# Kernel optimization log

Hardware: AMD Instinct MI355X
Metric: run time of the kernel (lower is better)

Reference implementation:

```python
import jax, jax.numpy as jnp
import numpy as np

N = 50000      # nodes
DEG = 12       # in-degree per node
E = N * DEG    # 600000 edges
IN_FEATS = 256
H_FEATS = 128
NUM_LAYERS = 2
BN_EPS = 1e-5
PD_EPS = 1e-6  # torch pairwise_distance eps


def _batch_norm(x):
    # BatchNorm1d(affine=False) in training mode: per-feature batch stats, biased var
    m = x.mean(axis=0)
    v = ((x - m) ** 2).mean(axis=0)
    return (x - m) / jnp.sqrt(v + BN_EPS)


def setup_inputs() -> dict:
    key = jax.random.key(0)
    ks = jax.random.split(key, 6)
    x = jax.random.normal(ks[0], (N, IN_FEATS), dtype=jnp.float32)
    # xavier-uniform-like scales
    s_init = float(np.sqrt(6.0 / (IN_FEATS + H_FEATS)))
    s_h = float(np.sqrt(6.0 / (2 * H_FEATS)))
    W_init = jax.random.uniform(ks[1], (IN_FEATS, H_FEATS), jnp.float32, -s_init, s_init)
    W0 = jax.random.uniform(ks[2], (H_FEATS, H_FEATS), jnp.float32, -s_h, s_h)
    W1 = jax.random.uniform(ks[3], (H_FEATS, H_FEATS), jnp.float32, -s_h, s_h)
    b0 = jnp.zeros((H_FEATS,), jnp.float32)
    b1 = jnp.zeros((H_FEATS,), jnp.float32)
    src = jax.random.randint(ks[4], (E,), 0, N, dtype=jnp.int32)
    dst = jnp.repeat(jnp.arange(N, dtype=jnp.int32), DEG)  # every node has in-degree DEG
    return {"x": x, "W_init": W_init, "W0": W0, "b0": b0, "W1": W1, "b1": b1,
            "src": src, "dst": dst}


def _embed_nodes(x, W_init, Ws, bs, src, dst):
    # h = act(norm(x @ init_weight)); then GraphConv(norm='none') layers
    h = jax.nn.relu(_batch_norm(x @ W_init))
    for W, b in zip(Ws, bs):
        msg = h[src] @ W                       # [E, H]
        agg = jax.ops.segment_sum(msg, dst, num_segments=N)  # sum aggregation
        h = jax.nn.relu(_batch_norm(agg + b))
    return h


def _nonparametric_embedding(x, src, dst, deg):
    # GIN(apply_func=None, eps=-1, aggregator='mean') == mean of in-neighbors
    h = jax.nn.relu(_batch_norm(x))
    for _ in range(NUM_LAYERS):
        agg = jax.ops.segment_sum(h[src], dst, num_segments=N) / deg[:, None]
        h = jax.nn.relu(_batch_norm(agg))
    return h


def _mean_edge_dist(h, src, dst, deg):
    # apply_edges: pairwise_distance(src, dst); pull: scatter-mean onto dst
    d = jnp.linalg.norm(h[src] - h[dst] + PD_EPS, axis=1)  # [E]
    return jax.ops.segment_sum(d, dst, num_segments=N) / deg  # [N]


def reference(x, W_init, W0, b0, W1, b1, src, dst):
    deg = jnp.maximum(
        jax.ops.segment_sum(jnp.ones((E,), jnp.float32), dst, num_segments=N), 1.0)
    h_final = _embed_nodes(x, W_init, (W0, W1), (b0, b1), src, dst)
    # nonparametric target distances (detached in original)
    h_nonpar = _nonparametric_embedding(jax.lax.stop_gradient(x), src, dst, deg)
    d_nonpar = jax.lax.stop_gradient(_mean_edge_dist(h_nonpar, src, dst, deg))
    d_par = _mean_edge_dist(h_final, src, dst, deg)
    loss = jnp.mean((jnp.log(d_par) - jnp.log(d_nonpar)) ** 2)
    return (h_final, loss)
```

## Files before the change

### kernel.cpp

```cpp
#include <hip/hip_runtime.h>
#include <hip/hip_fp16.h>
#include <math.h>

#define DEG 12
#define BN_EPS 1e-5f
#define PD_EPS 1e-6f

using uint = unsigned int;

typedef _Float16 fp16x8 __attribute__((ext_vector_type(8)));
typedef float f32x2 __attribute__((ext_vector_type(2)));
typedef float f32x4 __attribute__((ext_vector_type(4)));

__device__ inline float2 h2f2(uint u) {
  __half2 h; __builtin_memcpy(&h, &u, 4);
  return __half22float2(h);
}
__device__ inline uint f2h2(float a, float b) {
  __half2 h = __floats2half2_rn(a, b);
  uint u; __builtin_memcpy(&u, &h, 4);
  return u;
}
__device__ inline f32x2 q2f_lo(uint u) { return __builtin_amdgcn_cvt_pk_f32_fp8(u, false); }
__device__ inline f32x2 q2f_hi(uint u) { return __builtin_amdgcn_cvt_pk_f32_fp8(u, true); }
__device__ inline uint f4_to_q(float a, float b, float c, float d) {
  uint w = 0;
  w = __builtin_amdgcn_cvt_pk_fp8_f32(a, b, w, false);
  w = __builtin_amdgcn_cvt_pk_fp8_f32(c, d, w, true);
  return w;
}

#define STATS_NB 256

template<int F>
__global__ __launch_bounds__(512) void stats_h_part(const __half* __restrict__ in,
                                                    float* __restrict__ parts, int M) {
  const int G = F / 8;
  __shared__ float redA[512 * 8];
  __shared__ float redB[512 * 8];
  int tid = threadIdx.x;
  int total = M * G;
  float s[8] = {0,0,0,0,0,0,0,0}, q[8] = {0,0,0,0,0,0,0,0};
  for (int i = blockIdx.x * 512 + tid; i < total; i += gridDim.x * 512) {
    uint4 raw = ((const uint4*)in)[i];
    float2 v0 = h2f2(raw.x), v1 = h2f2(raw.y), v2 = h2f2(raw.z), v3 = h2f2(raw.w);
    float v[8] = {v0.x, v0.y, v1.x, v1.y, v2.x, v2.y, v3.x, v3.y};
#pragma unroll
    for (int j = 0; j < 8; ++j) { s[j] += v[j]; q[j] += v[j] * v[j]; }
  }
#pragma unroll
  for (int j = 0; j < 8; ++j) { redA[tid * 8 + j] = s[j]; redB[tid * 8 + j] = q[j]; }
  __syncthreads();
  if (tid < F) {
    int c = tid >> 3, j = tid & 7;
    float as = 0.f, aq = 0.f;
#pragma unroll 4
    for (int r = 0; r < 512 / G; ++r) {
      as += redA[(r * G + c) * 8 + j];
      aq += redB[(r * G + c) * 8 + j];
    }
    parts[blockIdx.x * 2 * F + tid]     = as;
    parts[blockIdx.x * 2 * F + F + tid] = aq;
  }
}

template<int F>
__global__ __launch_bounds__(512) void stats_q_part(const uint* __restrict__ in,
                                                    float* __restrict__ parts, int M) {
  const int G = F / 8;
  __shared__ float redA[512 * 8];
  __shared__ float redB[512 * 8];
  int tid = threadIdx.x;
  int total = M * G;
  float s[8] = {0,0,0,0,0,0,0,0}, q[8] = {0,0,0,0,0,0,0,0};
  for (int i = blockIdx.x * 512 + tid; i < total; i += gridDim.x * 512) {
    uint2 raw = ((const uint2*)in)[i];
    f32x2 a = q2f_lo(raw.x), b = q2f_hi(raw.x), c = q2f_lo(raw.y), d = q2f_hi(raw.y);
    float v[8] = {a.x, a.y, b.x, b.y, c.x, c.y, d.x, d.y};
#pragma unroll
    for (int j = 0; j < 8; ++j) { s[j] += v[j]; q[j] += v[j] * v[j]; }
  }
#pragma unroll
  for (int j = 0; j < 8; ++j) { redA[tid * 8 + j] = s[j]; redB[tid * 8 + j] = q[j]; }
  __syncthreads();
  if (tid < F) {
    int c = tid >> 3, j = tid & 7;
    float as = 0.f, aq = 0.f;
#pragma unroll 4
    for (int r = 0; r < 512 / G; ++r) {
      as += redA[(r * G + c) * 8 + j];
      aq += redB[(r * G + c) * 8 + j];
    }
    parts[blockIdx.x * 2 * F + tid]     = as;
    parts[blockIdx.x * 2 * F + F + tid] = aq;
  }
}

template<int F>
__global__ __launch_bounds__(512) void stats_f_part(const float* __restrict__ in,
                                                    float* __restrict__ parts, int M) {
  const int G = F / 4;
  __shared__ float redA[512 * 4];
  __shared__ float redB[512 * 4];
  int tid = threadIdx.x;
  int total = M * G;
  float s[4] = {0,0,0,0}, q[4] = {0,0,0,0};
  for (int i = blockIdx.x * 512 + tid; i < total; i += gridDim.x * 512) {
    float4 v = ((const float4*)in)[i];
    float w[4] = {v.x, v.y, v.z, v.w};
#pragma unroll
    for (int j = 0; j < 4; ++j) { s[j] += w[j]; q[j] += w[j] * w[j]; }
  }
#pragma unroll
  for (int j = 0; j < 4; ++j) { redA[tid * 4 + j] = s[j]; redB[tid * 4 + j] = q[j]; }
  __syncthreads();
  if (tid < F) {
    int c = tid >> 2, j = tid & 3;
    float as = 0.f, aq = 0.f;
#pragma unroll 4
    for (int r = 0; r < 512 / G; ++r) {
      as += redA[(r * G + c) * 4 + j];
      aq += redB[(r * G + c) * 4 + j];
    }
    parts[blockIdx.x * 2 * F + tid]     = as;
    parts[blockIdx.x * 2 * F + F + tid] = aq;
  }
}

template<int F>
__global__ __launch_bounds__(1024) void stats_final(const float* __restrict__ parts,
                                                    int M, float* __restrict__ stats) {
  const int OUT = 2 * F;
  const int T   = 1024 / OUT;
  __shared__ float red[1024];
  int tid = threadIdx.x;
  int o = tid & (OUT - 1);
  int c = tid / OUT;
  float s = 0.f;
#pragma unroll 16
  for (int b = c; b < STATS_NB; b += T) s += parts[b * OUT + o];
  red[tid] = s;
  __syncthreads();
  if (tid < OUT) {
    float acc = red[tid];
#pragma unroll
    for (int cc = 1; cc < T; ++cc) acc += red[cc * OUT + tid];
    red[tid] = acc;
  }
  __syncthreads();
  if (tid < F) {
    float mean = red[tid] / (float)M;
    float var  = red[F + tid] / (float)M - mean * mean;
    stats[tid]     = mean;
    stats[F + tid] = 1.0f / sqrtf(var + BN_EPS);
  }
}

__global__ void transpose_cast(const float* __restrict__ W, __half* __restrict__ WT, int K) {
  int idx = blockIdx.x * 256 + threadIdx.x;
  if (idx >= 128 * K) return;
  int n = idx / K, k = idx - n * K;
  WT[idx] = __float2half(W[(size_t)k * 128 + n]);
}

__global__ __launch_bounds__(256) void gemm_x(
    const float* __restrict__ A, const __half* __restrict__ WT,
    __half* __restrict__ C, int M) {
  int wave = threadIdx.x >> 6, lane = threadIdx.x & 63;
  int row0 = blockIdx.x * 64 + wave * 16;
  if (row0 >= M) return;
  int r  = lane & 15;
  int kg = lane >> 4;
  const float* Ap = A + (size_t)(row0 + r) * 256 + kg * 8;

  fp16x8 af[8];
#pragma unroll
  for (int a = 0; a < 8; ++a) {
    float4 lo = *(const float4*)(Ap + a * 32);
    float4 hi = *(const float4*)(Ap + a * 32 + 4);
    af[a][0] = (_Float16)lo.x; af[a][1] = (_Float16)lo.y;
    af[a][2] = (_Float16)lo.z; af[a][3] = (_Float16)lo.w;
    af[a][4] = (_Float16)hi.x; af[a][5] = (_Float16)hi.y;
    af[a][6] = (_Float16)hi.z; af[a][7] = (_Float16)hi.w;
  }
  f32x4 acc[8];
#pragma unroll
  for (int n = 0; n < 8; ++n) acc[n] = (f32x4){0.f, 0.f, 0.f, 0.f};
  const _Float16* WTh = (const _Float16*)WT;
#pragma unroll
  for (int a = 0; a < 8; ++a) {
#pragma unroll
    for (int n = 0; n < 8; ++n) {
      fp16x8 bf = *(const fp16x8*)(WTh + (size_t)(n * 16 + r) * 256 + kg * 8 + a * 32);
      acc[n] = __builtin_amdgcn_mfma_f32_16x16x32_f16(af[a], bf, acc[n], 0, 0, 0);
    }
  }
#pragma unroll
  for (int n = 0; n < 8; ++n) {
    int col = n * 16 + r;
#pragma unroll
    for (int rr = 0; rr < 4; ++rr) {
      int row = row0 + kg * 4 + rr;
      if (row < M) C[(size_t)row * 128 + col] = __float2half(acc[n][rr]);
    }
  }
}

template<bool OUT_HALF>
__global__ __launch_bounds__(256) void gemm_128(
    const __half* __restrict__ A, const __half* __restrict__ WT,
    const float* __restrict__ bias, void* __restrict__ Cv, int M) {
  int wave = threadIdx.x >> 6, lane = threadIdx.x & 63;
  int row0 = blockIdx.x * 64 + wave * 16;
  if (row0 >= M) return;
  int r  = lane & 15;
  int kg = lane >> 4;
  const _Float16* Ap = (const _Float16*)A + (size_t)(row0 + r) * 128 + kg * 8;

  fp16x8 af[4];
#pragma unroll
  for (int a = 0; a < 4; ++a) af[a] = *(const fp16x8*)(Ap + a * 32);

  f32x4 acc[8];
#pragma unroll
  for (int n = 0; n < 8; ++n) acc[n] = (f32x4){0.f, 0.f, 0.f, 0.f};
  const _Float16* WTh = (const _Float16*)WT;
#pragma unroll
  for (int a = 0; a < 4; ++a) {
#pragma unroll
    for (int n = 0; n < 8; ++n) {
      fp16x8 bf = *(const fp16x8*)(WTh + (size_t)(n * 16 + r) * 128 + kg * 8 + a * 32);
      acc[n] = __builtin_amdgcn_mfma_f32_16x16x32_f16(af[a], bf, acc[n], 0, 0, 0);
    }
  }
#pragma unroll
  for (int n = 0; n < 8; ++n) {
    int col = n * 16 + r;
    float bv = bias[col];
#pragma unroll
    for (int rr = 0; rr < 4; ++rr) {
      int row = row0 + kg * 4 + rr;
      if (row >= M) continue;
      float v = acc[n][rr] + bv;
      if (OUT_HALF) ((__half*)Cv)[(size_t)row * 128 + col] = __float2half(v);
      else          ((float*)Cv)[(size_t)row * 128 + col] = v;
    }
  }
}

template<int F, bool BNRELU>
__global__ __launch_bounds__(256) void agg_n(
    const __half* __restrict__ H, const float* __restrict__ stats,
    const int* __restrict__ src, __half* __restrict__ outh,
    float scale, int n_nodes) {
  const int LPN = F / 8;
  const int NPB = 256 / LPN;
  int tid  = threadIdx.x;
  int g    = tid / LPN;
  int lig  = tid % LPN;
  int node = blockIdx.x * NPB + g;
  if (node >= n_nodes) return;
  float m[8], iv[8];
  if (BNRELU) {
#pragma unroll
    for (int j = 0; j < 8; ++j) {
      m[j]  = stats[lig * 8 + j];
      iv[j] = stats[F + lig * 8 + j];
    }
  }
  int lane = tid & 63;
  int grpStart = lane & (63 ^ (LPN - 1));
  int se = 0;
  if ((lane & (LPN - 1)) < DEG) se = src[node * DEG + (lane & (LPN - 1))];

  const uint4* HH = (const uint4*)H;
  float a[8] = {0,0,0,0,0,0,0,0};
#pragma unroll
  for (int e = 0; e < DEG; ++e) {
    int s = __shfl(se, grpStart + e);
    uint4 raw = HH[(size_t)s * LPN + lig];
    float2 v0 = h2f2(raw.x), v1 = h2f2(raw.y), v2 = h2f2(raw.z), v3 = h2f2(raw.w);
    float w[8] = {v0.x, v0.y, v1.x, v1.y, v2.x, v2.y, v3.x, v3.y};
    if (BNRELU) {
#pragma unroll
      for (int j = 0; j < 8; ++j) w[j] = fmaxf((w[j] - m[j]) * iv[j], 0.f);
    }
#pragma unroll
    for (int j = 0; j < 8; ++j) a[j] += w[j];
  }
  uint4 w;
  w.x = f2h2(a[0] * scale, a[1] * scale);
  w.y = f2h2(a[2] * scale, a[3] * scale);
  w.z = f2h2(a[4] * scale, a[5] * scale);
  w.w = f2h2(a[6] * scale, a[7] * scale);
  ((uint4*)outh)[(size_t)node * LPN + lig] = w;
}

template<int F, bool BNRELU>
__global__ __launch_bounds__(256) void agg_q(
    const uint* __restrict__ H, const float* __restrict__ stats,
    const int* __restrict__ src, uint* __restrict__ outq,
    float scale, int n_nodes) {
  const int LPN = F / 8;
  const int NPB = 256 / LPN;
  int tid  = threadIdx.x;
  int g    = tid / LPN;
  int lig  = tid % LPN;
  int node = blockIdx.x * NPB + g;
  if (node >= n_nodes) return;
  float m[8], iv[8];
  if (BNRELU) {
#pragma unroll
    for (int j = 0; j < 8; ++j) {
      m[j]  = stats[lig * 8 + j];
      iv[j] = stats[F + lig * 8 + j];
    }
  }
  int lane = tid & 63;
  int grpStart = lane & (63 ^ (LPN - 1));
  int se = 0;
  if ((lane & (LPN - 1)) < DEG) se = src[node * DEG + (lane & (LPN - 1))];

  const uint2* HH = (const uint2*)H;
  float a[8] = {0,0,0,0,0,0,0,0};
#pragma unroll
  for (int e = 0; e < DEG; ++e) {
    int s = __shfl(se, grpStart + e);
    uint2 raw = HH[(size_t)s * LPN + lig];
    f32x2 p0 = q2f_lo(raw.x), p1 = q2f_hi(raw.x), p2 = q2f_lo(raw.y), p3 = q2f_hi(raw.y);
    float w[8] = {p0.x, p0.y, p1.x, p1.y, p2.x, p2.y, p3.x, p3.y};
    if (BNRELU) {
#pragma unroll
      for (int j = 0; j < 8; ++j) w[j] = fmaxf((w[j] - m[j]) * iv[j], 0.f);
    }
#pragma unroll
    for (int j = 0; j < 8; ++j) a[j] += w[j];
  }
  uint2 w;
  w.x = f4_to_q(a[0] * scale, a[1] * scale, a[2] * scale, a[3] * scale);
  w.y = f4_to_q(a[4] * scale, a[5] * scale, a[6] * scale, a[7] * scale);
  ((uint2*)outq)[(size_t)node * LPN + lig] = w;
}

template<int F>
__global__ __launch_bounds__(256) void dist_q(
    const uint* __restrict__ H, const int* __restrict__ src,
    float* __restrict__ out, int n_nodes) {
  const int LPN = 16;
  const int NPB = 256 / LPN;
  const int NU2 = F / 128;
  int tid  = threadIdx.x;
  int g    = tid / LPN;
  int lig  = tid % LPN;
  int node = blockIdx.x * NPB + g;
  if (node >= n_nodes) return;
  int lane = tid & 63;
  int grpStart = lane & 48;
  int se = 0;
  if ((lane & 15) < DEG) se = src[node * DEG + (lane & 15)];

  const uint2* HH = (const uint2*)H;
  float oe[NU2 * 8];
#pragma unroll
  for (int k = 0; k < NU2; ++k) {
    uint2 o = HH[(size_t)node * (F / 8) + lig * NU2 + k];
    f32x2 p0 = q2f_lo(o.x), p1 = q2f_hi(o.x), p2 = q2f_lo(o.y), p3 = q2f_hi(o.y);
    oe[k*8+0] = PD_EPS - p0.x; oe[k*8+1] = PD_EPS - p0.y;
    oe[k*8+2] = PD_EPS - p1.x; oe[k*8+3] = PD_EPS - p1.y;
    oe[k*8+4] = PD_EPS - p2.x; oe[k*8+5] = PD_EPS - p2.y;
    oe[k*8+6] = PD_EPS - p3.x; oe[k*8+7] = PD_EPS - p3.y;
  }

  float dsum = 0.f;
#pragma unroll
  for (int e = 0; e < DEG; ++e) {
    int s = __shfl(se, grpStart + e);
    float sq = 0.f;
#pragma unroll
    for (int k = 0; k < NU2; ++k) {
      uint2 raw = HH[(size_t)s * (F / 8) + lig * NU2 + k];
      f32x2 p0 = q2f_lo(raw.x), p1 = q2f_hi(raw.x), p2 = q2f_lo(raw.y), p3 = q2f_hi(raw.y);
      float w[8] = {p0.x, p0.y, p1.x, p1.y, p2.x, p2.y, p3.x, p3.y};
#pragma unroll
      for (int j = 0; j < 8; ++j) {
        float d = w[j] + oe[k*8+j];
        sq = fmaf(d, d, sq);
      }
    }
#pragma unroll
    for (int mask = 1; mask < LPN; mask <<= 1) sq += __shfl_xor(sq, mask);
    dsum += sqrtf(sq);
  }
  if (lig == 0) out[node] = dsum * (1.0f / (float)DEG);
}

template<int F>
__global__ void bnrelu_to_fp8(const float* __restrict__ in, const float* __restrict__ stats,
                              uint* __restrict__ out, int total4) {
  for (int idx = blockIdx.x * blockDim.x + threadIdx.x; idx < total4;
       idx += gridDim.x * blockDim.x) {
    float4 v = ((const float4*)in)[idx];
    int f0 = (idx & (F / 4 - 1)) * 4;
    float w0 = fmaxf((v.x - stats[f0+0]) * stats[F+f0+0], 0.f);
    float w1 = fmaxf((v.y - stats[f0+1]) * stats[F+f0+1], 0.f);
    float w2 = fmaxf((v.z - stats[f0+2]) * stats[F+f0+2], 0.f);
    float w3 = fmaxf((v.w - stats[f0+3]) * stats[F+f0+3], 0.f);
    out[idx] = f4_to_q(w0, w1, w2, w3);
  }
}

template<int F>
__global__ void bnrelu_q2q(const uint* __restrict__ in, const float* __restrict__ stats,
                           uint* __restrict__ out, int total1) {
  for (int idx = blockIdx.x * blockDim.x + threadIdx.x; idx < total1;
       idx += gridDim.x * blockDim.x) {
    uint raw = in[idx];
    int f0 = (idx & (F / 4 - 1)) * 4;
    f32x2 p0 = q2f_lo(raw), p1 = q2f_hi(raw);
    float w0 = fmaxf((p0.x - stats[f0+0]) * stats[F+f0+0], 0.f);
    float w1 = fmaxf((p0.y - stats[f0+1]) * stats[F+f0+1], 0.f);
    float w2 = fmaxf((p1.x - stats[f0+2]) * stats[F+f0+2], 0.f);
    float w3 = fmaxf((p1.y - stats[f0+3]) * stats[F+f0+3], 0.f);
    out[idx] = f4_to_q(w0, w1, w2, w3);
  }
}

template<int F>
__global__ void bnrelu_dual(const float* __restrict__ in, const float* __restrict__ stats,
                            float* __restrict__ outf, uint* __restrict__ outq, int total4) {
  for (int idx = blockIdx.x * blockDim.x + threadIdx.x; idx < total4;
       idx += gridDim.x * blockDim.x) {
    float4 v = ((const float4*)in)[idx];
    int f0 = (idx & (F / 4 - 1)) * 4;
    float w0 = fmaxf((v.x - stats[f0+0]) * stats[F+f0+0], 0.f);
    float w1 = fmaxf((v.y - stats[f0+1]) * stats[F+f0+1], 0.f);
    float w2 = fmaxf((v.z - stats[f0+2]) * stats[F+f0+2], 0.f);
    float w3 = fmaxf((v.w - stats[f0+3]) * stats[F+f0+3], 0.f);
    ((float4*)outf)[idx] = make_float4(w0, w1, w2, w3);
    outq[idx] = f4_to_q(w0, w1, w2, w3);
  }
}

__global__ void loss_partial(const float* __restrict__ dpar, const float* __restrict__ dnp,
                             float* __restrict__ parts, int n) {
  __shared__ float red[256];
  float acc = 0.f;
  for (int i = blockIdx.x * 256 + threadIdx.x; i < n; i += gridDim.x * 256) {
    float t = logf(dpar[i]) - logf(dnp[i]);
    acc += t * t;
  }
  red[threadIdx.x] = acc;
  __syncthreads();
  for (int s = 128; s; s >>= 1) {
    if (threadIdx.x < s) red[threadIdx.x] += red[threadIdx.x + s];
    __syncthreads();
  }
  if (threadIdx.x == 0) parts[blockIdx.x] = red[0];
}

__global__ void loss_final(const float* __restrict__ parts, int nb,
                           float* __restrict__ out, float inv_n) {
  if (threadIdx.x == 0) {
    float s = 0.f;
    for (int i = 0; i < nb; ++i) s += parts[i];
    *out = s * inv_n;
  }
}

extern "C" void kernel_launch(void* const* d_in, const int* in_sizes, int n_in,
                              void* d_out, int out_size, void* d_ws, size_t ws_size,
                              hipStream_t stream) {
  const float* x  = (const float*)d_in[0];
  const float* Wi = (const float*)d_in[1];
  const float* W0 = (const float*)d_in[2];
  const float* b0 = (const float*)d_in[3];
  const float* W1 = (const float*)d_in[4];
  const float* b1 = (const float*)d_in[5];
  const int*  src = (const int*)d_in[6];

  const int N = in_sizes[0] / 256;
  float* out = (float*)d_out;

  const size_t NF = (size_t)N * 128;
  float* S1 = (float*)d_ws;
  float* S2 = S1 + NF;
  float* S3 = S2 + NF;
  float* aux = S3 + NF;
  float* dpar   = aux;
  float* dnp    = dpar + N;
  float* parts  = dnp + N;
  float* s_x    = parts + STATS_NB * 512;
  float* s_y0   = s_x + 512;
  float* s_z1   = s_y0 + 256;
  float* s_z2   = s_z1 + 256;
  float* s_a1   = s_z2 + 256;
  float* s_a2   = s_a1 + 512;
  float* lparts = s_a2 + 512;
  __half* WiT   = (__half*)(lparts + 64);
  __half* W0T   = (__half*)(lparts + 64 + 16384);
  __half* W1T   = (__half*)(lparts + 64 + 24576);

  __half* y0h = (__half*)S1;
  __half* H0h = (__half*)S2;
  __half* z1h = (__half*)S1;
  __half* H1h = (__half*)S2;
  float*  z2  = S3;
  uint* hq   = (uint*)S1;
  uint* xq   = (uint*)S2;
  uint* A1q  = (uint*)S3;
  uint* A2q  = (uint*)S2;
  uint* A2nq = (uint*)S1;

  const int g64   = (N + 63) / 64;
  const int g128a = N / 16;
  const int gaggq = N / 8;
  const int gdist = N / 16;

  transpose_cast<<<(128 * 256 + 255) / 256, 256, 0, stream>>>(Wi, WiT, 256);
  transpose_cast<<<(128 * 128 + 255) / 256, 256, 0, stream>>>(W0, W0T, 128);
  transpose_cast<<<(128 * 128 + 255) / 256, 256, 0, stream>>>(W1, W1T, 128);

  gemm_x<<<g64, 256, 0, stream>>>(x, WiT, y0h, N);
  stats_h_part<128><<<STATS_NB, 512, 0, stream>>>(y0h, parts, N);
  stats_final<128><<<1, 1024, 0, stream>>>(parts, N, s_y0);
  agg_n<128, true><<<g128a, 256, 0, stream>>>(y0h, s_y0, src, H0h, 1.0f, N);
  gemm_128<true><<<g64, 256, 0, stream>>>(H0h, W0T, b0, z1h, N);
  stats_h_part<128><<<STATS_NB, 512, 0, stream>>>(z1h, parts, N);
  stats_final<128><<<1, 1024, 0, stream>>>(parts, N, s_z1);
  agg_n<128, true><<<g128a, 256, 0, stream>>>(z1h, s_z1, src, H1h, 1.0f, N);
  gemm_128<false><<<g64, 256, 0, stream>>>(H1h, W1T, b1, z2, N);
  stats_f_part<128><<<STATS_NB, 512, 0, stream>>>(z2, parts, N);
  stats_final<128><<<1, 1024, 0, stream>>>(parts, N, s_z2);
  bnrelu_dual<128><<<2048, 256, 0, stream>>>(z2, s_z2, out, hq, N * 32);
  dist_q<128><<<gdist, 256, 0, stream>>>(hq, src, dpar, N);

  stats_f_part<256><<<STATS_NB, 512, 0, stream>>>(x, parts, N);
  stats_final<256><<<1, 1024, 0, stream>>>(parts, N, s_x);
  bnrelu_to_fp8<256><<<2048, 256, 0, stream>>>(x, s_x, xq, N * 64);
  agg_q<256, false><<<gaggq, 256, 0, stream>>>(xq, nullptr, src, A1q, 1.0f / DEG, N);
  stats_q_part<256><<<STATS_NB, 512, 0, stream>>>(A1q, parts, N);
  stats_final<256><<<1, 1024, 0, stream>>>(parts, N, s_a1);
  agg_q<256, true><<<gaggq, 256, 0, stream>>>(A1q, s_a1, src, A2q, 1.0f / DEG, N);
  stats_q_part<256><<<STATS_NB, 512, 0, stream>>>(A2q, parts, N);
  stats_final<256><<<1, 1024, 0, stream>>>(parts, N, s_a2);
  bnrelu_q2q<256><<<2048, 256, 0, stream>>>(A2q, s_a2, A2nq, N * 64);
  dist_q<256><<<gdist, 256, 0, stream>>>(A2nq, src, dnp, N);

  loss_partial<<<64, 256, 0, stream>>>(dpar, dnp, lparts, N);
  loss_final<<<1, 64, 0, stream>>>(lparts, 64, out + (size_t)N * 128, 1.0f / (float)N);
}
```

Before: 324.2 us.

## Fuse x batchnorm-relu fp8 quantization into first GEMM and stage weights in LDS

Moves the statistics pass over x ahead of the first GEMM so that gemm_x can also apply batchnorm plus ReLU and write the fp8 copy of x while it already holds the rows. This removes the separate bnrelu_to_fp8 pass and its second full read of the 50000x256 fp32 input. Both GEMM kernels now load the transposed weight matrix into swizzled shared memory once per block instead of each wave fetching it from global memory. The xq buffer gets its own workspace region because the S2 slot it used before is now still live when it is written. The cost is extra barriers, more LDS use that may reduce occupancy, and a longer first GEMM.

Measured after the change: 277.2 us. 14.5% less time.

```diff
diff --git a/kernel.cpp b/kernel.cpp
--- a/kernel.cpp
+++ b/kernel.cpp
@@ -164,35 +164,70 @@
 }
 
 __global__ __launch_bounds__(256) void gemm_x(
-    const float* __restrict__ A, const __half* __restrict__ WT,
-    __half* __restrict__ C, int M) {
-  int wave = threadIdx.x >> 6, lane = threadIdx.x & 63;
+    const float* __restrict__ A, const float* __restrict__ stats,
+    const __half* __restrict__ WT, __half* __restrict__ C,
+    uint* __restrict__ xq, int M) {
+  __shared__ uint4 Bs4[64 * 32];
+  char* Bs = (char*)Bs4;
+  int tid = threadIdx.x;
+  int wave = tid >> 6, lane = tid & 63;
   int row0 = blockIdx.x * 64 + wave * 16;
-  if (row0 >= M) return;
-  int r  = lane & 15;
-  int kg = lane >> 4;
-  const float* Ap = A + (size_t)(row0 + r) * 256 + kg * 8;
+  int r = lane & 15, kg = lane >> 4;
+  int arow = row0 + r; if (arow >= M) arow = M - 1;
+  bool vrow = (row0 + r) < M;
+  const float* Ap = A + (size_t)arow * 256 + kg * 8;
 
   fp16x8 af[8];
 #pragma unroll
   for (int a = 0; a < 8; ++a) {
+    int c0 = kg * 8 + a * 32;
     float4 lo = *(const float4*)(Ap + a * 32);
     float4 hi = *(const float4*)(Ap + a * 32 + 4);
     af[a][0] = (_Float16)lo.x; af[a][1] = (_Float16)lo.y;
     af[a][2] = (_Float16)lo.z; af[a][3] = (_Float16)lo.w;
     af[a][4] = (_Float16)hi.x; af[a][5] = (_Float16)hi.y;
     af[a][6] = (_Float16)hi.z; af[a][7] = (_Float16)hi.w;
-  }
+    float4 m0 = *(const float4*)(stats + c0);
+    float4 m1 = *(const float4*)(stats + c0 + 4);
+    float4 v0 = *(const float4*)(stats + 256 + c0);
+    float4 v1 = *(const float4*)(stats + 256 + c0 + 4);
+    float w0 = fmaxf((lo.x - m0.x) * v0.x, 0.f);
+    float w1 = fmaxf((lo.y - m0.y) * v0.y, 0.f);
+    float w2 = fmaxf((lo.z - m0.z) * v0.z, 0.f);
+    float w3 = fmaxf((lo.w - m0.w) * v0.w, 0.f);
+    float w4 = fmaxf((hi.x - m1.x) * v1.x, 0.f);
+    float w5 = fmaxf((hi.y - m1.y) * v1.y, 0.f);
+    float w6 = fmaxf((hi.z - m1.z) * v1.z, 0.f);
+    float w7 = fmaxf((hi.w - m1.w) * v1.w, 0.f);
+    if (vrow) {
+      uint2 q; q.x = f4_to_q(w0, w1, w2, w3); q.y = f4_to_q(w4, w5, w6, w7);
+      ((uint2*)xq)[(size_t)arow * 32 + (c0 >> 3)] = q;
+    }
+  }
+
   f32x4 acc[8];
 #pragma unroll
   for (int n = 0; n < 8; ++n) acc[n] = (f32x4){0.f, 0.f, 0.f, 0.f};
-  const _Float16* WTh = (const _Float16*)WT;
-#pragma unroll
-  for (int a = 0; a < 8; ++a) {
-#pragma unroll
-    for (int n = 0; n < 8; ++n) {
-      fp16x8 bf = *(const fp16x8*)(WTh + (size_t)(n * 16 + r) * 256 + kg * 8 + a * 32);
-      acc[n] = __builtin_amdgcn_mfma_f32_16x16x32_f16(af[a], bf, acc[n], 0, 0, 0);
+  const uint4* Wg = (const uint4*)WT;
+
+#pragma unroll
+  for (int ph = 0; ph < 2; ++ph) {
+    __syncthreads();
+#pragma unroll
+    for (int i = 0; i < 8; ++i) {
+      int idx = tid + i * 256;
+      int rw = idx >> 5, c16 = idx & 31;
+      *(uint4*)(Bs + rw * 512 + ((c16 * 16) ^ ((rw & 7) << 4))) = Wg[ph * 2048 + idx];
+    }
+    __syncthreads();
+#pragma unroll
+    for (int a = 0; a < 8; ++a) {
+#pragma unroll
+      for (int n4 = 0; n4 < 4; ++n4) {
+        int rw = n4 * 16 + r;
+        fp16x8 bf = *(const fp16x8*)(Bs + rw * 512 + ((kg * 16 + a * 64) ^ ((r & 7) << 4)));
+        acc[ph * 4 + n4] = __builtin_amdgcn_mfma_f32_16x16x32_f16(af[a], bf, acc[ph * 4 + n4], 0, 0, 0);
+      }
     }
   }
 #pragma unroll
@@ -210,26 +245,36 @@
 __global__ __launch_bounds__(256) void gemm_128(
     const __half* __restrict__ A, const __half* __restrict__ WT,
     const float* __restrict__ bias, void* __restrict__ Cv, int M) {
-  int wave = threadIdx.x >> 6, lane = threadIdx.x & 63;
+  __shared__ uint4 Bs4[128 * 16];
+  char* Bs = (char*)Bs4;
+  int tid = threadIdx.x;
+  const uint4* Wg = (const uint4*)WT;
+#pragma unroll
+  for (int i = 0; i < 8; ++i) {
+    int idx = tid + i * 256;
+    int rw = idx >> 4, c16 = idx & 15;
+    *(uint4*)(Bs + rw * 256 + ((c16 * 16) ^ ((rw & 7) << 4))) = Wg[idx];
+  }
+  int wave = tid >> 6, lane = tid & 63;
   int row0 = blockIdx.x * 64 + wave * 16;
-  if (row0 >= M) return;
-  int r  = lane & 15;
-  int kg = lane >> 4;
-  const _Float16* Ap = (const _Float16*)A + (size_t)(row0 + r) * 128 + kg * 8;
+  int r = lane & 15, kg = lane >> 4;
+  int arow = row0 + r; if (arow >= M) arow = M - 1;
+  const _Float16* Ap = (const _Float16*)A + (size_t)arow * 128 + kg * 8;
 
   fp16x8 af[4];
 #pragma unroll
   for (int a = 0; a < 4; ++a) af[a] = *(const fp16x8*)(Ap + a * 32);
 
+  __syncthreads();
   f32x4 acc[8];
 #pragma unroll
   for (int n = 0; n < 8; ++n) acc[n] = (f32x4){0.f, 0.f, 0.f, 0.f};
-  const _Float16* WTh = (const _Float16*)WT;
 #pragma unroll
   for (int a = 0; a < 4; ++a) {
 #pragma unroll
     for (int n = 0; n < 8; ++n) {
-      fp16x8 bf = *(const fp16x8*)(WTh + (size_t)(n * 16 + r) * 128 + kg * 8 + a * 32);
+      int rw = n * 16 + r;
+      fp16x8 bf = *(const fp16x8*)(Bs + rw * 256 + ((kg * 16 + a * 64) ^ ((r & 7) << 4)));
       acc[n] = __builtin_amdgcn_mfma_f32_16x16x32_f16(af[a], bf, acc[n], 0, 0, 0);
     }
   }
@@ -392,21 +437,6 @@
     dsum += sqrtf(sq);
   }
   if (lig == 0) out[node] = dsum * (1.0f / (float)DEG);
-}
-
-template<int F>
-__global__ void bnrelu_to_fp8(const float* __restrict__ in, const float* __restrict__ stats,
-                              uint* __restrict__ out, int total4) {
-  for (int idx = blockIdx.x * blockDim.x + threadIdx.x; idx < total4;
-       idx += gridDim.x * blockDim.x) {
-    float4 v = ((const float4*)in)[idx];
-    int f0 = (idx & (F / 4 - 1)) * 4;
-    float w0 = fmaxf((v.x - stats[f0+0]) * stats[F+f0+0], 0.f);
-    float w1 = fmaxf((v.y - stats[f0+1]) * stats[F+f0+1], 0.f);
-    float w2 = fmaxf((v.z - stats[f0+2]) * stats[F+f0+2], 0.f);
-    float w3 = fmaxf((v.w - stats[f0+3]) * stats[F+f0+3], 0.f);
-    out[idx] = f4_to_q(w0, w1, w2, w3);
-  }
 }
 
 template<int F>
@@ -499,6 +529,7 @@
   __half* WiT   = (__half*)(lparts + 64);
   __half* W0T   = (__half*)(lparts + 64 + 16384);
   __half* W1T   = (__half*)(lparts + 64 + 24576);
+  uint*   xq    = (uint*)(lparts + 64 + 32768);
 
   __half* y0h = (__half*)S1;
   __half* H0h = (__half*)S2;
@@ -506,7 +537,6 @@
   __half* H1h = (__half*)S2;
   float*  z2  = S3;
   uint* hq   = (uint*)S1;
-  uint* xq   = (uint*)S2;
   uint* A1q  = (uint*)S3;
   uint* A2q  = (uint*)S2;
   uint* A2nq = (uint*)S1;
@@ -520,7 +550,10 @@
   transpose_cast<<<(128 * 128 + 255) / 256, 256, 0, stream>>>(W0, W0T, 128);
   transpose_cast<<<(128 * 128 + 255) / 256, 256, 0, stream>>>(W1, W1T, 128);
 
-  gemm_x<<<g64, 256, 0, stream>>>(x, WiT, y0h, N);
+  stats_f_part<256><<<STATS_NB, 512, 0, stream>>>(x, parts, N);
+  stats_final<256><<<1, 1024, 0, stream>>>(parts, N, s_x);
+
+  gemm_x<<<g64, 256, 0, stream>>>(x, s_x, WiT, y0h, xq, N);
   stats_h_part<128><<<STATS_NB, 512, 0, stream>>>(y0h, parts, N);
   stats_final<128><<<1, 1024, 0, stream>>>(parts, N, s_y0);
   agg_n<128, true><<<g128a, 256, 0, stream>>>(y0h, s_y0, src, H0h, 1.0f, N);
@@ -534,9 +567,6 @@
   bnrelu_dual<128><<<2048, 256, 0, stream>>>(z2, s_z2, out, hq, N * 32);
   dist_q<128><<<gdist, 256, 0, stream>>>(hq, src, dpar, N);
 
-  stats_f_part<256><<<STATS_NB, 512, 0, stream>>>(x, parts, N);
-  stats_final<256><<<1, 1024, 0, stream>>>(parts, N, s_x);
-  bnrelu_to_fp8<256><<<2048, 256, 0, stream>>>(x, s_x, xq, N * 64);
   agg_q<256, false><<<gaggq, 256, 0, stream>>>(xq, nullptr, src, A1q, 1.0f / DEG, N);
   stats_q_part<256><<<STATS_NB, 512, 0, stream>>>(A1q, parts, N);
   stats_final<256><<<1, 1024, 0, stream>>>(parts, N, s_a1);
```
